# Kernel optimization log

Hardware: AMD Instinct MI355X
Metric: run time of the kernel (lower is better)

Reference implementation:

```python
import jax, jax.numpy as jnp
import numpy as np

B, D, H = 4096, 64, 1024  # batch, state dim, hidden width


def setup_inputs() -> dict:
    key = jax.random.key(0)
    ks = jax.random.split(key, 4)
    def w(k, shape, fan_in):
        return (jax.random.normal(k, shape, jnp.float32) / np.float32(np.sqrt(fan_in)))
    return {
        "x": jax.random.normal(ks[0], (B, 1 + D), jnp.float32),
        "W1": w(ks[1], (D, H), D),
        "b1": jnp.zeros((H,), jnp.float32),
        "W2": w(ks[2], (H, H), H),
        "b2": jnp.zeros((H,), jnp.float32),
        "W3": w(ks[3], (H, D), H),
        "b3": jnp.zeros((D,), jnp.float32),
    }


def _mlp(z, W1, b1, W2, b2, W3, b3):
    # tanh MLP vector field: d -> h -> h -> d
    h = jnp.tanh(z @ W1 + b1)
    h = jnp.tanh(h @ W2 + b2)
    return h @ W3 + b3


def reference(x, W1, b1, W2, b2, W3, b3):
    x_in = x[:, 1:]                        # [B, D] state (col 0 is logp channel)
    f = lambda z: _mlp(z, W1, b1, W2, b2, W3, b3)
    x_out = f(x_in)                        # [B, D]

    # Exact Jacobian trace: same math as the torch per-dim autograd.grad loop,
    # expressed as D forward-mode JVPs vmapped over the identity basis.
    eye = jnp.eye(x_in.shape[1], dtype=x.dtype)

    def diag_entry(e):                     # e: [D] basis vector
        _, t = jax.jvp(f, (x_in,), (jnp.broadcast_to(e, x_in.shape),))
        return t @ e                       # [B] = J[:, i, i]

    trJ = jnp.sum(jax.vmap(diag_entry)(eye), axis=0)  # [B]

    out = jnp.concatenate([-trJ[:, None], x_out], axis=1)  # [B, 1+D]
    return out + 0.0 * x  # faithful to `+ 0 * x` in the original
```

## Files before the change

### kernel.cpp

```cpp
#include <hip/hip_runtime.h>
#include <cmath>

typedef unsigned short u16;
typedef __attribute__((ext_vector_type(8))) short s8v;
typedef __attribute__((ext_vector_type(4))) float f4v;
typedef __attribute__((ext_vector_type(16))) float f16v;

__device__ __forceinline__ u16 f2bf(float f) {
    union { float f; unsigned u; } v; v.f = f;
    unsigned r = v.u + 0x7FFFu + ((v.u >> 16) & 1u);
    return (u16)(r >> 16);
}
__device__ __forceinline__ float tanh_fast(float x) {
    float e = __builtin_amdgcn_exp2f(x * 2.88539008177792681f);
    return 1.f - 2.f * __builtin_amdgcn_rcpf(1.f + e);
}
__device__ __forceinline__ int wslot(int row, int c) {
    return ((((c >> 2) << 6) | ((c & 3) << 4) | (row & 15)) ^ c);
}
__device__ __forceinline__ size_t fragoff(int n, int k) {
    return (((size_t)(n >> 5) * 64 + (k >> 4)) * 64 + (n & 31) + (((k >> 3) & 1) << 5)) * 8 + (k & 7);
}

__launch_bounds__(256)
__global__ void cnf_prep(const float* __restrict__ x, const float* __restrict__ W1,
                         const float* __restrict__ W2, const float* __restrict__ W3,
                         u16* __restrict__ W2Tf, u16* __restrict__ VTf,
                         u16* __restrict__ xb, u16* __restrict__ W1T,
                         u16* __restrict__ W3Tf, float* __restrict__ trJ,
                         float* __restrict__ obuf)
{
    __shared__ float w2s[32][33];
    __shared__ __align__(16) float w1s[64][36];
    const int a = blockIdx.x * 32;
    const int b = blockIdx.y * 32;
    const int t = threadIdx.x;

    obuf[(blockIdx.y * 32 + blockIdx.x) * 256 + t] = 0.f;

    #pragma unroll
    for (int it = 0; it < 4; ++it) {
        int idx = t + it * 256;
        w2s[idx >> 5][idx & 31] = W2[(a + (idx >> 5)) * 1024 + b + (idx & 31)];
    }
    #pragma unroll
    for (int it = 0; it < 8; ++it) {
        int idx = t + it * 256;
        w1s[idx >> 5][idx & 31] = W1[(idx >> 5) * 1024 + a + (idx & 31)];
    }
    __syncthreads();

    #pragma unroll
    for (int it = 0; it < 4; ++it) {
        int idx = t + it * 256;
        int rr = idx >> 5, cc = idx & 31;
        W2Tf[fragoff(b + rr, a + cc)] = f2bf(w2s[cc][rr]);
    }
    {
        const int q = t >> 3, pg = t & 7;
        const float* w3row = W3 + (b + q) * 64;
        f4v u = f4v{0.f, 0.f, 0.f, 0.f};
        #pragma unroll
        for (int i4 = 0; i4 < 16; ++i4) {
            f4v w3v = *(const f4v*)&w3row[i4 * 4];
            #pragma unroll
            for (int s = 0; s < 4; ++s) {
                f4v wv = *(const f4v*)&w1s[i4 * 4 + s][pg * 4];
                u += w3v[s] * wv;
            }
        }
        #pragma unroll
        for (int j = 0; j < 4; ++j) {
            const int pp = pg * 4 + j;
            VTf[fragoff(b + q, a + pp)] = f2bf(w2s[pp][q] * u[j]);
        }
    }
    {
        int bid = blockIdx.y * 32 + blockIdx.x;
        int e = bid * 256 + t;
        xb[e] = f2bf(x[(e >> 6) * 65 + 1 + (e & 63)]);
    }
    if (blockIdx.y == 0) {
        int pp = t >> 3, i0 = (t & 7) * 8;
        s8v v;
        #pragma unroll
        for (int j = 0; j < 8; ++j) v[j] = (short)f2bf(w1s[i0 + j][pp]);
        *(s8v*)&W1T[(a + pp) * 64 + i0] = v;
        if (t < 128) trJ[blockIdx.x * 128 + t] = 0.f;
    }
    if (blockIdx.y == 1) {
        int idx = blockIdx.x * 256 + t;
        int n = idx & 63, k0 = (idx >> 6) * 8;
        s8v v;
        #pragma unroll
        for (int j = 0; j < 8; ++j) v[j] = (short)f2bf(W3[(k0 + j) * 64 + n]);
        *(s8v*)&W3Tf[fragoff(n, k0)] = v;
    }
}

__launch_bounds__(256)
__global__ void cnf_gemm1(const u16* __restrict__ xb, const u16* __restrict__ W1T,
                          const float* __restrict__ b1,
                          u16* __restrict__ h1f, u16* __restrict__ g1f)
{
    __shared__ __align__(16) u16 lds[12 * 1024];
    __shared__ __align__(16) u16 hls[128 * 64];
    __shared__ __align__(16) u16 gls[128 * 64];
    const int t = threadIdx.x;
    const int wave = t >> 6, lane = t & 63;
    const int wm = wave >> 1, wn = wave & 1;
    const int g = lane >> 4, lr = lane & 15;
    const int arow0 = blockIdx.x * 128, bcol0 = blockIdx.y * 64;

    #pragma unroll
    for (int i = 0; i < 4; ++i) {
        int ch = t + i * 256, row = ch >> 3, c = ch & 7;
        *(s8v*)&lds[(row >> 4) * 1024 + wslot(row, c) * 8] =
            *(const s8v*)&xb[(arow0 + row) * 64 + c * 8];
    }
    #pragma unroll
    for (int i = 0; i < 2; ++i) {
        int ch = t + i * 256, row = ch >> 3, c = ch & 7;
        *(s8v*)&lds[(8 + (row >> 4)) * 1024 + wslot(row, c) * 8] =
            *(const s8v*)&W1T[(bcol0 + row) * 64 + c * 8];
    }
    __syncthreads();

    f4v acc[4][2];
    #pragma unroll
    for (int mi = 0; mi < 4; ++mi)
        #pragma unroll
        for (int ni = 0; ni < 2; ++ni) acc[mi][ni] = f4v{0.f,0.f,0.f,0.f};

    #pragma unroll
    for (int ks = 0; ks < 2; ++ks) {
        const int lo = (ks * 64 + (lane ^ ((ks * 4 + g) & 7))) * 8;
        s8v af[4], bf[2];
        #pragma unroll
        for (int mi = 0; mi < 4; ++mi) af[mi] = *(const s8v*)&lds[(wm * 4 + mi) * 1024 + lo];
        #pragma unroll
        for (int ni = 0; ni < 2; ++ni) bf[ni] = *(const s8v*)&lds[(8 + wn * 2 + ni) * 1024 + lo];
        #pragma unroll
        for (int mi = 0; mi < 4; ++mi)
            #pragma unroll
            for (int ni = 0; ni < 2; ++ni)
                acc[mi][ni] = __builtin_amdgcn_mfma_f32_16x16x32_bf16(af[mi], bf[ni], acc[mi][ni], 0, 0, 0);
    }

    #pragma unroll
    for (int mi = 0; mi < 4; ++mi) {
        const int rowl = wm * 64 + mi * 16 + g * 4;
        #pragma unroll
        for (int ni = 0; ni < 2; ++ni) {
            const int coll = wn * 32 + ni * 16 + lr;
            const float bv = b1[bcol0 + coll];
            const int cc = coll >> 3, jj = coll & 7;
            #pragma unroll
            for (int r = 0; r < 4; ++r) {
                const int row = rowl + r;
                float h = tanh_fast(acc[mi][ni][r] + bv);
                int idx = row * 64 + ((cc ^ (row & 7)) << 3) + jj;
                hls[idx] = f2bf(h);
                gls[idx] = f2bf(1.f - h * h);
            }
        }
    }
    __syncthreads();

    const int rt0 = arow0 >> 5, kk0 = bcol0 >> 4;
    #pragma unroll
    for (int i = 0; i < 4; ++i) {
        const int tile = (i * 256 + t) >> 6;
        const int ln = t & 63;
        const int rt = tile >> 2, kk = tile & 3;
        const int row = rt * 32 + (ln & 31);
        const int kb = kk * 16 + (ln >> 5) * 8;
        const int src = row * 64 + (((kb >> 3) ^ (row & 7)) << 3);
        const size_t dst = ((size_t)(rt0 + rt) * 64 + (kk0 + kk)) * 512 + ln * 8;
        *(s8v*)&h1f[dst] = *(const s8v*)&hls[src];
        *(s8v*)&g1f[dst] = *(const s8v*)&gls[src];
    }
}

#define LOADB(B, kt)                                                           \
    do { _Pragma("unroll")                                                     \
         for (int _ks = 0; _ks < 2; ++_ks) {                                   \
             size_t _o = (((size_t)(ntb + wn) * 64 + (kt) * 2 + _ks) * 512) + lane * 8; \
             B[_ks*2 + 0] = *(const s8v*)&W2Tf[_o];                            \
             B[_ks*2 + 1] = *(const s8v*)&VTf[_o];                             \
         } } while (0)

#define MIDBODY(kt, AwH, AwG, AlH, AlG, Bc, Bn)                                \
    {                                                                          \
        const u16* _buf = &lds[(kt) & 1][0];                                   \
        s8v a1[2][2], a2[2][2];                                  \
        _Pragma("unroll")                                                      \
        for (int ks = 0; ks < 2; ++ks)                                         \
            _Pragma("unroll")                                                  \
            for (int mt = 0; mt < 2; ++mt) {                                   \
                const int f = ((wrt * 2 + mt) * 2 + ks) * 512 + lane * 8;      \
                a1[ks][mt] = *(const s8v*)&_buf[f];                            \
                a2[ks][mt] = *(const s8v*)&_buf[4096 + f];                     \
            }                                                                  \
        if ((kt) < 30) {                                                       \
            const size_t _go = (size_t)((kt) + 2) * 1024;                      \
            AlH = *(const s8v*)(h1f + sg0 + _go);                              \
            AlG = *(const s8v*)(g1f + sg0 + _go);                              \
        }                                                                      \
        if ((kt) < 31) {                                                       \
            u16* _wb = &lds[((kt) + 1) & 1][0];                                \
            *(s8v*)&_wb[sd0] = AwH; *(s8v*)&_wb[4096 + sd0] = AwG;             \
            LOADB(Bn, (kt) + 1);                                               \
        }                                                                      \
        _Pragma("unroll")                                                      \
        for (int ks = 0; ks < 2; ++ks)                                         \
            _Pragma("unroll")                                                  \
            for (int mt = 0; mt < 2; ++mt) {                                   \
                acc1[mt] = __builtin_amdgcn_mfma_f32_32x32x16_bf16(a1[ks][mt], Bc[ks*2+0], acc1[mt], 0, 0, 0); \
                acc2[mt] = __builtin_amdgcn_mfma_f32_32x32x16_bf16(a2[ks][mt], Bc[ks*2+1], acc2[mt], 0, 0, 0); \
            }                                                                  \
        __syncthreads();                                                       \
    }

__launch_bounds__(512, 1)
__global__ void cnf_mid(const u16* __restrict__ h1f, const u16* __restrict__ g1f,
                        const u16* __restrict__ W2Tf, const u16* __restrict__ VTf,
                        const u16* __restrict__ W3Tf,
                        const float* __restrict__ b2, const float* __restrict__ b3,
                        float* __restrict__ obuf, float* __restrict__ trJ)
{
    __shared__ __align__(16) u16 lds[2][8192];

    const int t = threadIdx.x;
    const int wave = t >> 6, lane = t & 63;
    const int wrt = wave & 1;
    const int wn  = wave >> 1;
    const int bx = blockIdx.x;
    const int by = blockIdx.y;
    const int arow0 = bx * 128;
    const int ntb = by * 4;

    const int lc8 = (t & 63) * 8;
    const int rt_s = t >> 7, kk_s = (t >> 6) & 1;
    const size_t sg0 = ((size_t)(bx * 4 + rt_s) * 64 + kk_s) * 512 + lc8;
    const int sd0 = (rt_s * 2 + kk_s) * 512 + lc8;

    f16v acc1[2], acc2[2];
    #pragma unroll
    for (int mt = 0; mt < 2; ++mt)
        #pragma unroll
        for (int r = 0; r < 16; ++r) { acc1[mt][r] = 0.f; acc2[mt][r] = 0.f; }

    s8v raH, raG, rbH, rbG;
    s8v bA[4], bB[4];

    raH = *(const s8v*)(h1f + sg0);
    raG = *(const s8v*)(g1f + sg0);
    {
        u16* wb = &lds[0][0];
        *(s8v*)&wb[sd0] = raH; *(s8v*)&wb[4096 + sd0] = raG;
    }
    raH = *(const s8v*)(h1f + sg0 + 1024);
    raG = *(const s8v*)(g1f + sg0 + 1024);
    LOADB(bA, 0);
    __syncthreads();

    for (int kt2 = 0; kt2 < 16; ++kt2) {
        const int kt = kt2 * 2;
        MIDBODY(kt,     raH, raG, rbH, rbG, bA, bB);
        MIDBODY(kt + 1, rbH, rbG, raH, raG, bB, bA);
    }

    u16* hls = &lds[0][0];
    const int l31 = lane & 31, lh = lane >> 5;
    #pragma unroll
    for (int mt = 0; mt < 2; ++mt) {
        const int coll = wn * 32 + l31;
        const float bv = b2[by * 128 + coll];
        float tr[16];
        #pragma unroll
        for (int r = 0; r < 16; ++r) {
            float hh = tanh_fast(acc1[mt][r] + bv);
            float gg = 1.f - hh * hh;
            const int row = wrt * 64 + mt * 32 + (r & 3) + ((r >> 2) << 3) + lh * 4;
            hls[row * 128 + (((coll >> 3) ^ (row & 15)) << 3) + (coll & 7)] = f2bf(hh);
            tr[r] = acc2[mt][r] * gg;
        }
        #pragma unroll
        for (int off = 1; off < 32; off <<= 1)
            #pragma unroll
            for (int r = 0; r < 16; ++r) tr[r] += __shfl_xor(tr[r], off);
        if (l31 == 0) {
            const int rowb = arow0 + (wrt * 2 + mt) * 32 + lh * 4;
            #pragma unroll
            for (int r = 0; r < 16; ++r)
                atomicAdd(&trJ[rowb + (r & 3) + ((r >> 2) << 3)], tr[r]);
        }
    }
    __syncthreads();

    {
        const int ort = wave & 3, ont = wave >> 2;
        f16v oacc;
        #pragma unroll
        for (int r = 0; r < 16; ++r) oacc[r] = 0.f;
        #pragma unroll
        for (int kk = 0; kk < 8; ++kk) {
            const int row = ort * 32 + l31;
            const int ch = (kk * 2 + lh) ^ (row & 15);
            s8v af = *(const s8v*)&hls[row * 128 + ch * 8];
            s8v bf = *(const s8v*)&W3Tf[((size_t)ont * 64 + by * 8 + kk) * 512 + lane * 8];
            oacc = __builtin_amdgcn_mfma_f32_32x32x16_bf16(af, bf, oacc, 0, 0, 0);
        }
        const int col = ont * 32 + l31;
        const float badd = (by == 0) ? b3[col] : 0.f;
        #pragma unroll
        for (int r = 0; r < 16; ++r) {
            const int row = arow0 + ort * 32 + (r & 3) + ((r >> 2) << 3) + lh * 4;
            atomicAdd(&obuf[(size_t)row * 64 + col], oacc[r] + badd);
        }
    }
}

__launch_bounds__(256)
__global__ void cnf_fin(const float* __restrict__ obuf, const float* __restrict__ trJ,
                        float* __restrict__ out)
{
    const int t = threadIdx.x;
    const int row0 = blockIdx.x * 16;
    const int c = t & 63, rr = t >> 6;
    #pragma unroll
    for (int i = 0; i < 4; ++i) {
        const int row = row0 + rr + i * 4;
        out[(size_t)row * 65 + 1 + c] = obuf[(size_t)row * 64 + c];
    }
    if (t < 16) out[(size_t)(row0 + t) * 65] = -trJ[row0 + t];
}

extern "C" void kernel_launch(void* const* d_in, const int* in_sizes, int n_in,
                              void* d_out, int out_size, void* d_ws, size_t ws_size,
                              hipStream_t stream) {
    const float* x  = (const float*)d_in[0];
    const float* W1 = (const float*)d_in[1];
    const float* b1 = (const float*)d_in[2];
    const float* W2 = (const float*)d_in[3];
    const float* b2 = (const float*)d_in[4];
    const float* W3 = (const float*)d_in[5];
    const float* b3 = (const float*)d_in[6];
    float* out = (float*)d_out;

    char* ws = (char*)d_ws;
    u16*   h1f = (u16*)(ws);
    u16*   g1f = (u16*)(ws + (size_t)( 8u << 20));
    float* obf = (float*)(ws + (size_t)(16u << 20));
    u16*   W2T = (u16*)(ws + (size_t)(24u << 20));
    u16*   VTb = (u16*)(ws + (size_t)(26u << 20));
    float* trJ = (float*)(ws + (size_t)(28u << 20));
    u16*   xbb = (u16*)(ws + (size_t)(28u << 20) + 65536);
    u16*   W1T = (u16*)(ws + (size_t)(28u << 20) + 65536 + 524288);
    u16*   W3T = (u16*)(ws + (size_t)(28u << 20) + 65536 + 524288 + 131072);

    cnf_prep <<<dim3(32, 32), 256, 0, stream>>>(x, W1, W2, W3, W2T, VTb, xbb, W1T, W3T, trJ, obf);
    cnf_gemm1<<<dim3(32, 16), 256, 0, stream>>>(xbb, W1T, b1, h1f, g1f);
    cnf_mid  <<<dim3(32, 8),  512, 0, stream>>>(h1f, g1f, W2T, VTb, W3T, b2, b3, obf, trJ);
    cnf_fin  <<<256,          256, 0, stream>>>(obf, trJ, out);
}
```

Baseline: 57.82 us.

## Restructure mid GEMM with direct global-to-LDS loads and smaller 128x64 tiles

Rewrites the middle kernel so each block computes a 128x64 output tile with 4 waves instead of 128x128 with 8 waves, doubling the grid to 512 blocks. Both A (h1/g1) and B (W2/V) fragments are staged through LDS with global_load_lds DMA instructions rather than register round-trips, and the register-level double buffering is dropped in favour of a simple load-sync-compute-sync loop. The intent is higher occupancy, fewer VGPRs and less load issue overhead. The cost is lost overlap between loads and MFMA work, and more atomic traffic from the extra column blocks into obuf and trJ.

After: 66.10 us. 14.3% more time.

```diff
diff --git a/kernel.cpp b/kernel.cpp
--- a/kernel.cpp
+++ b/kernel.cpp
@@ -20,6 +20,12 @@
 }
 __device__ __forceinline__ size_t fragoff(int n, int k) {
     return (((size_t)(n >> 5) * 64 + (k >> 4)) * 64 + (n & 31) + (((k >> 3) & 1) << 5)) * 8 + (k & 7);
+}
+__device__ __forceinline__ void gload_lds16(const u16* g, u16* l) {
+    __builtin_amdgcn_global_load_lds(
+        (const __attribute__((address_space(1))) void*)g,
+        (__attribute__((address_space(3))) void*)l,
+        16, 0, 0);
 }
 
 __launch_bounds__(256)
@@ -182,54 +188,14 @@
     }
 }
 
-#define LOADB(B, kt)                                                           \
-    do { _Pragma("unroll")                                                     \
-         for (int _ks = 0; _ks < 2; ++_ks) {                                   \
-             size_t _o = (((size_t)(ntb + wn) * 64 + (kt) * 2 + _ks) * 512) + lane * 8; \
-             B[_ks*2 + 0] = *(const s8v*)&W2Tf[_o];                            \
-             B[_ks*2 + 1] = *(const s8v*)&VTf[_o];                             \
-         } } while (0)
-
-#define MIDBODY(kt, AwH, AwG, AlH, AlG, Bc, Bn)                                \
-    {                                                                          \
-        const u16* _buf = &lds[(kt) & 1][0];                                   \
-        s8v a1[2][2], a2[2][2];                                  \
-        _Pragma("unroll")                                                      \
-        for (int ks = 0; ks < 2; ++ks)                                         \
-            _Pragma("unroll")                                                  \
-            for (int mt = 0; mt < 2; ++mt) {                                   \
-                const int f = ((wrt * 2 + mt) * 2 + ks) * 512 + lane * 8;      \
-                a1[ks][mt] = *(const s8v*)&_buf[f];                            \
-                a2[ks][mt] = *(const s8v*)&_buf[4096 + f];                     \
-            }                                                                  \
-        if ((kt) < 30) {                                                       \
-            const size_t _go = (size_t)((kt) + 2) * 1024;                      \
-            AlH = *(const s8v*)(h1f + sg0 + _go);                              \
-            AlG = *(const s8v*)(g1f + sg0 + _go);                              \
-        }                                                                      \
-        if ((kt) < 31) {                                                       \
-            u16* _wb = &lds[((kt) + 1) & 1][0];                                \
-            *(s8v*)&_wb[sd0] = AwH; *(s8v*)&_wb[4096 + sd0] = AwG;             \
-            LOADB(Bn, (kt) + 1);                                               \
-        }                                                                      \
-        _Pragma("unroll")                                                      \
-        for (int ks = 0; ks < 2; ++ks)                                         \
-            _Pragma("unroll")                                                  \
-            for (int mt = 0; mt < 2; ++mt) {                                   \
-                acc1[mt] = __builtin_amdgcn_mfma_f32_32x32x16_bf16(a1[ks][mt], Bc[ks*2+0], acc1[mt], 0, 0, 0); \
-                acc2[mt] = __builtin_amdgcn_mfma_f32_32x32x16_bf16(a2[ks][mt], Bc[ks*2+1], acc2[mt], 0, 0, 0); \
-            }                                                                  \
-        __syncthreads();                                                       \
-    }
-
-__launch_bounds__(512, 1)
+__launch_bounds__(256)
 __global__ void cnf_mid(const u16* __restrict__ h1f, const u16* __restrict__ g1f,
                         const u16* __restrict__ W2Tf, const u16* __restrict__ VTf,
                         const u16* __restrict__ W3Tf,
                         const float* __restrict__ b2, const float* __restrict__ b3,
                         float* __restrict__ obuf, float* __restrict__ trJ)
 {
-    __shared__ __align__(16) u16 lds[2][8192];
+    __shared__ __align__(16) u16 lds[12288];
 
     const int t = threadIdx.x;
     const int wave = t >> 6, lane = t & 63;
@@ -238,12 +204,19 @@
     const int bx = blockIdx.x;
     const int by = blockIdx.y;
     const int arow0 = bx * 128;
-    const int ntb = by * 4;
-
-    const int lc8 = (t & 63) * 8;
-    const int rt_s = t >> 7, kk_s = (t >> 6) & 1;
-    const size_t sg0 = ((size_t)(bx * 4 + rt_s) * 64 + kk_s) * 512 + lc8;
-    const int sd0 = (rt_s * 2 + kk_s) * 512 + lc8;
+
+    const u16* src[6];
+    #pragma unroll
+    for (int i = 0; i < 6; ++i) {
+        const int fid = wave * 6 + i;
+        const u16* base; int rt;
+        if (fid < 8)       { base = h1f;  rt = bx * 4 + (fid >> 1); }
+        else if (fid < 16) { base = g1f;  rt = bx * 4 + ((fid - 8) >> 1); }
+        else if (fid < 20) { base = W2Tf; rt = by * 2 + ((fid - 16) >> 1); }
+        else               { base = VTf;  rt = by * 2 + ((fid - 20) >> 1); }
+        src[i] = base + ((size_t)rt * 64 + (fid & 1)) * 512 + lane * 8;
+    }
+    u16* const dstw = &lds[wave * 6 * 512];
 
     f16v acc1[2], acc2[2];
     #pragma unroll
@@ -251,39 +224,43 @@
         #pragma unroll
         for (int r = 0; r < 16; ++r) { acc1[mt][r] = 0.f; acc2[mt][r] = 0.f; }
 
-    s8v raH, raG, rbH, rbG;
-    s8v bA[4], bB[4];
-
-    raH = *(const s8v*)(h1f + sg0);
-    raG = *(const s8v*)(g1f + sg0);
-    {
-        u16* wb = &lds[0][0];
-        *(s8v*)&wb[sd0] = raH; *(s8v*)&wb[4096 + sd0] = raG;
-    }
-    raH = *(const s8v*)(h1f + sg0 + 1024);
-    raG = *(const s8v*)(g1f + sg0 + 1024);
-    LOADB(bA, 0);
-    __syncthreads();
-
-    for (int kt2 = 0; kt2 < 16; ++kt2) {
-        const int kt = kt2 * 2;
-        MIDBODY(kt,     raH, raG, rbH, rbG, bA, bB);
-        MIDBODY(kt + 1, rbH, rbG, raH, raG, bB, bA);
-    }
-
-    u16* hls = &lds[0][0];
+    const int lo = lane * 8;
+    for (int kt = 0; kt < 32; ++kt) {
+        #pragma unroll
+        for (int i = 0; i < 6; ++i)
+            gload_lds16(src[i] + (size_t)kt * 1024, dstw + i * 512);
+        __syncthreads();
+
+        #pragma unroll
+        for (int ks = 0; ks < 2; ++ks) {
+            s8v b1v = *(const s8v*)&lds[(16 + wn * 2 + ks) * 512 + lo];
+            s8v b2v = *(const s8v*)&lds[(20 + wn * 2 + ks) * 512 + lo];
+            #pragma unroll
+            for (int mt = 0; mt < 2; ++mt) {
+                const int fa = ((wrt * 2 + mt) * 2 + ks) * 512 + lo;
+                s8v a1 = *(const s8v*)&lds[fa];
+                s8v a2 = *(const s8v*)&lds[4096 + fa];
+                acc1[mt] = __builtin_amdgcn_mfma_f32_32x32x16_bf16(a1, b1v, acc1[mt], 0, 0, 0);
+                acc2[mt] = __builtin_amdgcn_mfma_f32_32x32x16_bf16(a2, b2v, acc2[mt], 0, 0, 0);
+            }
+        }
+        __syncthreads();
+    }
+
+    u16* hls = &lds[0];
     const int l31 = lane & 31, lh = lane >> 5;
     #pragma unroll
     for (int mt = 0; mt < 2; ++mt) {
         const int coll = wn * 32 + l31;
-        const float bv = b2[by * 128 + coll];
+        const float bv = b2[by * 64 + coll];
+        const int cc = coll >> 3, jj = coll & 7;
         float tr[16];
         #pragma unroll
         for (int r = 0; r < 16; ++r) {
             float hh = tanh_fast(acc1[mt][r] + bv);
             float gg = 1.f - hh * hh;
             const int row = wrt * 64 + mt * 32 + (r & 3) + ((r >> 2) << 3) + lh * 4;
-            hls[row * 128 + (((coll >> 3) ^ (row & 15)) << 3) + (coll & 7)] = f2bf(hh);
+            hls[row * 64 + ((cc ^ (row & 7)) << 3) + jj] = f2bf(hh);
             tr[r] = acc2[mt][r] * gg;
         }
         #pragma unroll
@@ -300,24 +277,32 @@
     __syncthreads();
 
     {
-        const int ort = wave & 3, ont = wave >> 2;
-        f16v oacc;
-        #pragma unroll
-        for (int r = 0; r < 16; ++r) oacc[r] = 0.f;
-        #pragma unroll
-        for (int kk = 0; kk < 8; ++kk) {
+        const int ort = wave;
+        f16v oacc[2];
+        #pragma unroll
+        for (int ni = 0; ni < 2; ++ni)
+            #pragma unroll
+            for (int r = 0; r < 16; ++r) oacc[ni][r] = 0.f;
+        #pragma unroll
+        for (int kk = 0; kk < 4; ++kk) {
             const int row = ort * 32 + l31;
-            const int ch = (kk * 2 + lh) ^ (row & 15);
-            s8v af = *(const s8v*)&hls[row * 128 + ch * 8];
-            s8v bf = *(const s8v*)&W3Tf[((size_t)ont * 64 + by * 8 + kk) * 512 + lane * 8];
-            oacc = __builtin_amdgcn_mfma_f32_32x32x16_bf16(af, bf, oacc, 0, 0, 0);
-        }
-        const int col = ont * 32 + l31;
-        const float badd = (by == 0) ? b3[col] : 0.f;
-        #pragma unroll
-        for (int r = 0; r < 16; ++r) {
-            const int row = arow0 + ort * 32 + (r & 3) + ((r >> 2) << 3) + lh * 4;
-            atomicAdd(&obuf[(size_t)row * 64 + col], oacc[r] + badd);
+            const int ch = (kk * 2 + lh) ^ (row & 7);
+            s8v af = *(const s8v*)&hls[row * 64 + ch * 8];
+            #pragma unroll
+            for (int ni = 0; ni < 2; ++ni) {
+                s8v bf = *(const s8v*)&W3Tf[((size_t)ni * 64 + by * 4 + kk) * 512 + lane * 8];
+                oacc[ni] = __builtin_amdgcn_mfma_f32_32x32x16_bf16(af, bf, oacc[ni], 0, 0, 0);
+            }
+        }
+        #pragma unroll
+        for (int ni = 0; ni < 2; ++ni) {
+            const int col = ni * 32 + l31;
+            const float badd = (by == 0) ? b3[col] : 0.f;
+            #pragma unroll
+            for (int r = 0; r < 16; ++r) {
+                const int row = arow0 + ort * 32 + (r & 3) + ((r >> 2) << 3) + lh * 4;
+                atomicAdd(&obuf[(size_t)row * 64 + col], oacc[ni][r] + badd);
+            }
         }
     }
 }
@@ -362,6 +347,6 @@
 
     cnf_prep <<<dim3(32, 32), 256, 0, stream>>>(x, W1, W2, W3, W2T, VTb, xbb, W1T, W3T, trJ, obf);
     cnf_gemm1<<<dim3(32, 16), 256, 0, stream>>>(xbb, W1T, b1, h1f, g1f);
-    cnf_mid  <<<dim3(32, 8),  512, 0, stream>>>(h1f, g1f, W2T, VTb, W3T, b2, b3, obf, trJ);
+    cnf_mid  <<<dim3(32, 16), 256, 0, stream>>>(h1f, g1f, W2T, VTb, W3T, b2, b3, obf, trJ);
     cnf_fin  <<<256,          256, 0, stream>>>(obf, trJ, out);
 }
```
